# Optimization experiments

Measured on AMD Instinct MI355X. Metric: run time of the kernel, lower is better.

Reference implementation:

```python
import jax, jax.numpy as jnp
from jax import lax
import numpy as np

# pywt db4 filter bank (ascending order)
DEC_LO = np.array([-0.010597401784997278, 0.032883011666982945, 0.030841381835986965,
                   -0.18703481171888114, -0.02798376941698385, 0.6308807679295904,
                   0.7148465705525415, 0.23037781330885523], dtype=np.float32)
F_LEN = DEC_LO.shape[0]
_signs = ((-1.0) ** (np.arange(F_LEN) + 1)).astype(np.float32)
DEC_HI = _signs * DEC_LO[::-1]
REC_LO = DEC_LO[::-1].copy()
REC_HI = DEC_HI[::-1].copy()
# conv filters flipped -> cross-correlation kernels for lax.conv
DEC_K = np.stack([DEC_LO[::-1], DEC_HI[::-1]])[:, None, :]   # (2, 1, F): lo/hi analysis
REC_K = np.stack([REC_LO[::-1], REC_HI[::-1]])[None, :, :]   # (1, 2, F): synthesis, sums lo+hi
LEVELS = 3


def dwt_level(x, dec_k):
    """One symmetric-mode DWT level. x: (M, n) -> (cA, cD) each (M, floor((n+F-1)/2))."""
    f = dec_k.shape[-1]
    x_ext = jnp.pad(x, ((0, 0), (f - 1, f - 1)), mode='symmetric')[:, 1:]
    y = lax.conv_general_dilated(x_ext[:, None, :], dec_k, (2,), 'VALID',
                                 dimension_numbers=('NCH', 'OIH', 'NCH'))
    return y[:, 0], y[:, 1]


def idwt_level(ca, cd, rec_k, out_len):
    """One IDWT level; trims to out_len (original length at that level)."""
    f = rec_k.shape[-1]
    m, L = ca.shape
    up = jnp.zeros((m, 2, 2 * L), ca.dtype).at[:, 0, ::2].set(ca).at[:, 1, ::2].set(cd)
    y = lax.conv_general_dilated(up, rec_k, (1,), [(f - 1, f - 1)],
                                 dimension_numbers=('NCH', 'OIH', 'NCH'))[:, 0]
    s = f - 2
    return y[:, s:s + out_len]


def setup_inputs() -> dict:
    key = jax.random.key(0)
    B, N, D = 8, 4096, 768
    x = jax.random.normal(key, (B, N, D), dtype=jnp.float32)
    w_approx = jnp.ones((D,), dtype=jnp.float32)
    w_details = jnp.ones((LEVELS, D), dtype=jnp.float32)
    return {"x": x, "w_approx": w_approx, "w_details": w_details}


def reference(x, w_approx, w_details):
    B, N, D = x.shape
    dec_k = jnp.asarray(DEC_K)
    rec_k = jnp.asarray(REC_K)
    # all channels processed at once: (B, N, D) -> (B*D, N)
    sig = x.transpose(0, 2, 1).reshape(B * D, N)
    # J-level decomposition, recording per-level lengths for reconstruction
    a = sig
    lengths = []
    details = []
    for _ in range(LEVELS):
        lengths.append(a.shape[-1])
        a, d = dwt_level(a, dec_k)
        details.append(d)
    # pointwise mixing: one scalar per channel per band (matches ones(1,1,D) param sliced per-channel)
    def chan(w):  # (D,) -> (B*D, 1)
        return jnp.broadcast_to(w, (B, D)).reshape(B * D, 1)
    a = a * chan(w_approx)
    details = [d * chan(w_details[j]) for j, d in enumerate(details)]
    # reconstruction
    rec = a
    for j in reversed(range(LEVELS)):
        rec = idwt_level(rec, details[j], rec_k, lengths[j])
    rec = rec.reshape(B, D, N).transpose(0, 2, 1)
    # residual connection (dropout=0.0)
    return x + rec
```

## Files before the change

### kernel.cpp

```cpp
#include <hip/hip_runtime.h>


namespace {

constexpr int NT  = 256;
constexpr int N0  = 4096;
constexpr int DCH = 768;
constexpr int G   = 8;
constexpr int T   = 256;
constexpr int NTI = N0 / T;
constexpr int NDG = DCH / G;
constexpr int L1v = 2051, L2v = 1029, L3v = 518;

constexpr int SP   = 972;
constexpr int OX   = 0;
constexpr int OA1  = 356;
constexpr int OD1  = 536;
constexpr int OA2  = 716;
constexpr int OD2  = 804;
constexpr int OA3  = 892;
constexpr int OD3  = 932;
constexpr int OREC = 716;

__device__ constexpr float LO[8] = {
  -0.010597401784997278f,  0.032883011666982945f,  0.030841381835986965f,
  -0.18703481171888114f,  -0.02798376941698385f,   0.6308807679295904f,
   0.7148465705525415f,    0.23037781330885523f };
__device__ constexpr float HI[8] = {
  -0.23037781330885523f,   0.7148465705525415f,   -0.6308807679295904f,
  -0.02798376941698385f,   0.18703481171888114f,   0.030841381835986965f,
  -0.032883011666982945f, -0.010597401784997278f };
__device__ constexpr float LOF[8] = {
   0.23037781330885523f,   0.7148465705525415f,    0.6308807679295904f,
  -0.02798376941698385f,  -0.18703481171888114f,   0.030841381835986965f,
   0.032883011666982945f, -0.010597401784997278f };
__device__ constexpr float HIF[8] = {
  -0.010597401784997278f, -0.032883011666982945f,  0.030841381835986965f,
   0.18703481171888114f,  -0.02798376941698385f,  -0.6308807679295904f,
   0.7148465705525415f,   -0.23037781330885523f };

__device__ __forceinline__ int refl(int g, int n) {
  g = (g < 0) ? (-g - 1) : g;
  return (g >= n) ? (2 * n - 1 - g) : g;
}


template <int K>
__device__ __forceinline__ void analyze_v(const float* __restrict__ in,
                                          float* __restrict__ oa,
                                          float* __restrict__ od,
                                          int ntask, int i2) {
  for (int v = i2; v < ntask; v += 32) {
    float r[12];
#pragma unroll
    for (int j = 0; j < 3; ++j) {
      const float4 t = *reinterpret_cast<const float4*>(in + 4 * v + 4 * j);
      r[4 * j + 0] = t.x; r[4 * j + 1] = t.y;
      r[4 * j + 2] = t.z; r[4 * j + 3] = t.w;
    }
    float a0 = 0.f, h0 = 0.f, a1 = 0.f, h1 = 0.f;
#pragma unroll
    for (int k = 0; k < 8; ++k) {
      a0 = fmaf(LOF[k], r[K + k], a0);
      h0 = fmaf(HIF[k], r[K + k], h0);
      a1 = fmaf(LOF[k], r[K + 2 + k], a1);
      h1 = fmaf(HIF[k], r[K + 2 + k], h1);
    }
    *reinterpret_cast<float2*>(oa + 2 * v) = make_float2(a0, a1);
    *reinterpret_cast<float2*>(od + 2 * v) = make_float2(h0, h1);
  }
}

__device__ __forceinline__ void synth3_v(const float* __restrict__ pa,
                                         const float* __restrict__ pd,
                                         float* __restrict__ o, float sa,
                                         float sd, int ntask, int i2) {
  if (i2 < ntask) {
    const int u = i2;
    float ra[8], rd[8];
#pragma unroll
    for (int j = 0; j < 2; ++j) {
      const float4 t0 = *reinterpret_cast<const float4*>(pa + 4 * u + 4 * j);
      const float4 t1 = *reinterpret_cast<const float4*>(pd + 4 * u + 4 * j);
      ra[4*j+0] = t0.x; ra[4*j+1] = t0.y; ra[4*j+2] = t0.z; ra[4*j+3] = t0.w;
      rd[4*j+0] = t1.x; rd[4*j+1] = t1.y; rd[4*j+2] = t1.z; rd[4*j+3] = t1.w;
    }
    float ov[8];
#pragma unroll
    for (int tt = 0; tt < 4; ++tt) {
      float e = 0.f, ed = 0.f, oe = 0.f, od_ = 0.f;
#pragma unroll
      for (int m = 0; m < 4; ++m) {
        e   = fmaf(LO[2 * m + 1], ra[tt + m], e);
        ed  = fmaf(HI[2 * m + 1], rd[tt + m], ed);
        oe  = fmaf(LO[2 * m],     ra[tt + m], oe);
        od_ = fmaf(HI[2 * m],     rd[tt + m], od_);
      }
      ov[2 * tt]     = sa * e  + sd * ed;
      ov[2 * tt + 1] = sa * oe + sd * od_;
    }
    *reinterpret_cast<float4*>(o + 8 * u)     = make_float4(ov[0], ov[1], ov[2], ov[3]);
    *reinterpret_cast<float4*>(o + 8 * u + 4) = make_float4(ov[4], ov[5], ov[6], ov[7]);
  }
}

__device__ __forceinline__ void synth2_v(const float* __restrict__ pa,
                                         const float* __restrict__ pd,
                                         float* __restrict__ o, float sd,
                                         int ntask, int i2) {
  if (i2 < ntask) {
    const int u = i2;
    float ra[8], rd[12];
#pragma unroll
    for (int j = 0; j < 2; ++j) {
      const float4 t0 = *reinterpret_cast<const float4*>(pa + 4 * u + 4 * j);
      ra[4*j+0] = t0.x; ra[4*j+1] = t0.y; ra[4*j+2] = t0.z; ra[4*j+3] = t0.w;
    }
#pragma unroll
    for (int j = 0; j < 3; ++j) {
      const float4 t1 = *reinterpret_cast<const float4*>(pd + 4 * u + 4 + 4 * j);
      rd[4*j+0] = t1.x; rd[4*j+1] = t1.y; rd[4*j+2] = t1.z; rd[4*j+3] = t1.w;
    }
    float ov[8];
#pragma unroll
    for (int tt = 0; tt < 4; ++tt) {
      float e = 0.f, ed = 0.f, oe = 0.f, od_ = 0.f;
#pragma unroll
      for (int m = 0; m < 4; ++m) {
        e   = fmaf(LO[2 * m + 1], ra[tt + m], e);
        ed  = fmaf(HI[2 * m + 1], rd[tt + 2 + m], ed);
        oe  = fmaf(LO[2 * m],     ra[tt + m], oe);
        od_ = fmaf(HI[2 * m],     rd[tt + 2 + m], od_);
      }
      ov[2 * tt]     = e  + sd * ed;
      ov[2 * tt + 1] = oe + sd * od_;
    }
    *reinterpret_cast<float4*>(o + 8 * u)     = make_float4(ov[0], ov[1], ov[2], ov[3]);
    *reinterpret_cast<float4*>(o + 8 * u + 4) = make_float4(ov[4], ov[5], ov[6], ov[7]);
  }
}

__device__ __forceinline__ void final_v(const float* __restrict__ pa,
                                        const float* __restrict__ pd,
                                        const float* __restrict__ px,
                                        float* __restrict__ rec, float sd,
                                        int i2) {
  const int u = i2;
  float ra[8], rd[8], rx[12];
#pragma unroll
  for (int j = 0; j < 2; ++j) {
    const float4 t0 = *reinterpret_cast<const float4*>(pa + 4 * u + 4 * j);
    const float4 t1 = *reinterpret_cast<const float4*>(pd + 4 * u + 20 + 4 * j);
    ra[4*j+0] = t0.x; ra[4*j+1] = t0.y; ra[4*j+2] = t0.z; ra[4*j+3] = t0.w;
    rd[4*j+0] = t1.x; rd[4*j+1] = t1.y; rd[4*j+2] = t1.z; rd[4*j+3] = t1.w;
  }
#pragma unroll
  for (int j = 0; j < 3; ++j) {
    const float4 t2 = *reinterpret_cast<const float4*>(px + 8 * u + 44 + 4 * j);
    rx[4*j+0] = t2.x; rx[4*j+1] = t2.y; rx[4*j+2] = t2.z; rx[4*j+3] = t2.w;
  }
  float ov[8];
#pragma unroll
  for (int tt = 0; tt < 4; ++tt) {
    float e = 0.f, ed = 0.f, oe = 0.f, od_ = 0.f;
#pragma unroll
    for (int m = 0; m < 4; ++m) {
      e   = fmaf(LO[2 * m + 1], ra[tt + m], e);
      ed  = fmaf(HI[2 * m + 1], rd[tt + m], ed);
      oe  = fmaf(LO[2 * m],     ra[tt + m], oe);
      od_ = fmaf(HI[2 * m],     rd[tt + m], od_);
    }
    ov[2 * tt]     = e  + sd * ed  + rx[2 + 2 * tt];
    ov[2 * tt + 1] = oe + sd * od_ + rx[3 + 2 * tt];
  }
  *reinterpret_cast<float4*>(rec + 8 * u)     = make_float4(ov[0], ov[1], ov[2], ov[3]);
  *reinterpret_cast<float4*>(rec + 8 * u + 4) = make_float4(ov[4], ov[5], ov[6], ov[7]);
}


__device__ void analyze_g(const float* __restrict__ in, int Oin,
                          float* __restrict__ oa, float* __restrict__ od,
                          int cnt, int Oout, int lenout, int i2) {
  for (int p = i2; p < cnt; p += 32) {
    const int gp = refl(Oout + p, lenout);
    const int qb = 2 * gp - 6 - Oin;
    float alo = 0.f, ahi = 0.f;
#pragma unroll
    for (int k = 0; k < 8; ++k) {
      const float v = in[qb + k];
      alo = fmaf(LOF[k], v, alo);
      ahi = fmaf(HIF[k], v, ahi);
    }
    oa[p] = alo;
    od[p] = ahi;
  }
}

__device__ void synth_g(const float* __restrict__ ca,
                        const float* __restrict__ cd, int doff,
                        float* __restrict__ o, float sa, float sd, int npair,
                        int i2) {
  for (int t = i2; t < npair; t += 32) {
    float e = 0.f, ed = 0.f, oe = 0.f, od_ = 0.f;
#pragma unroll
    for (int m = 0; m < 4; ++m) {
      e   = fmaf(LO[2 * m + 1], ca[t + m], e);
      ed  = fmaf(HI[2 * m + 1], cd[t + doff + m], ed);
      oe  = fmaf(LO[2 * m],     ca[t + m], oe);
      od_ = fmaf(HI[2 * m],     cd[t + doff + m], od_);
    }
    o[2 * t]     = sa * e  + sd * ed;
    o[2 * t + 1] = sa * oe + sd * od_;
  }
}

}

__global__ __launch_bounds__(NT) void wavemix_kernel(
    const float* __restrict__ x, const float* __restrict__ wap,
    const float* __restrict__ wdet, float* __restrict__ out) {
  __shared__ float pool[G * SP];

  const int cpx = gridDim.x >> 3;
  const int wg  = (blockIdx.x & 7) * cpx + (blockIdx.x >> 3);
  const int nt   = wg & (NTI - 1);
  const int rest = wg >> 4;
  const int dg   = rest % NDG;
  const int b    = rest / NDG;
  const int n0   = nt * T;
  const int d0   = dg * G;
  const int tid  = threadIdx.x;
  const bool edge = (nt == 0) || (nt == NTI - 1);

  {
    const int q  = tid & 1;
    const int pl = tid >> 1;
    for (int p = pl; p < 352; p += 128) {
      int g = n0 - 46 + p;
      if (edge) g = refl(g, N0);
      const float4 v = *reinterpret_cast<const float4*>(
          x + ((size_t)b * N0 + g) * DCH + d0 + 4 * q);
      float* dst = pool + (4 * q) * SP + OX + p;
      dst[0]      = v.x;
      dst[SP]     = v.y;
      dst[2 * SP] = v.z;
      dst[3 * SP] = v.w;
    }
  }

  const int c2 = tid >> 5;
  const int i2 = tid & 31;
  float* P = pool + c2 * SP;
  const float wa = wap[d0 + c2];
  const float w2 = wdet[2 * DCH + d0 + c2];
  const float w1 = wdet[1 * DCH + d0 + c2];
  const float w0 = wdet[0 * DCH + d0 + c2];
  __syncthreads();

  if (!edge) {
    analyze_v<0>(P + OX,  P + OA1, P + OD1, 86, i2);
    __syncthreads();
    analyze_v<2>(P + OA1, P + OA2, P + OD2, 44, i2);
    __syncthreads();
    analyze_v<0>(P + OA2, P + OA3, P + OD3, 20, i2);
    __syncthreads();
    synth3_v(P + OA3, P + OD3, P + OA2, wa, w2, 9, i2);
    __syncthreads();
    synth2_v(P + OA2, P + OD2, P + OA1, w1, 17, i2);
    __syncthreads();
    final_v(P + OA1, P + OD1, P + OX, P + OREC, w0, i2);
  } else {
    analyze_g(P + OX,  n0 - 46,      P + OA1, P + OD1, 172, n0 / 2 - 20, L1v, i2);
    __syncthreads();
    analyze_g(P + OA1, n0 / 2 - 20,  P + OA2, P + OD2,  82, n0 / 4 - 6,  L2v, i2);
    __syncthreads();
    analyze_g(P + OA2, n0 / 4 - 6,   P + OA3, P + OD3,  38, n0 / 8,      L3v, i2);
    __syncthreads();
    synth_g(P + OA3, P + OD3, 0, P + OA2, wa,  w2, 35, i2);
    __syncthreads();
    synth_g(P + OA2, P + OD2, 6, P + OA1, 1.f, w1, 66, i2);
    __syncthreads();
    for (int t = i2; t < 128; t += 32) {
      const float* pa = P + OA1;
      const float* pd = P + OD1;
      float e = 0.f, ed = 0.f, oe = 0.f, od_ = 0.f;
#pragma unroll
      for (int m = 0; m < 4; ++m) {
        e   = fmaf(LO[2 * m + 1], pa[t + m], e);
        ed  = fmaf(HI[2 * m + 1], pd[t + 20 + m], ed);
        oe  = fmaf(LO[2 * m],     pa[t + m], oe);
        od_ = fmaf(HI[2 * m],     pd[t + 20 + m], od_);
      }
      (P + OREC)[2 * t]     = e  + w0 * ed  + (P + OX)[2 * t + 46];
      (P + OREC)[2 * t + 1] = oe + w0 * od_ + (P + OX)[2 * t + 47];
    }
  }
  __syncthreads();

  {
    const int c = tid & 7;
    const int j = tid >> 3;
    const float* R = pool + c * SP + OREC;
    float* orow = out + ((size_t)b * N0 + n0) * DCH + d0 + c;
    for (int pos = j; pos < T; pos += 32)
      orow[(size_t)pos * DCH] = R[pos];
  }
}

extern "C" void kernel_launch(void* const* d_in, const int* in_sizes, int n_in,
                              void* d_out, int out_size, void* d_ws, size_t ws_size,
                              hipStream_t stream) {
  const float* x  = (const float*)d_in[0];
  const float* wa = (const float*)d_in[1];
  const float* wd = (const float*)d_in[2];
  float* out      = (float*)d_out;

  const int B    = in_sizes[0] / (N0 * DCH);
  const int grid = B * NDG * NTI;
  wavemix_kernel<<<grid, NT, 0, stream>>>(x, wa, wd, out);
}
```

Before: 61.45 us.

## Replace shared-memory interior tiles with per-thread streaming register DWT pipeline

Interior tiles now give each thread one channel and stream along the sequence through a register-resident multi-level wavelet pipeline. Each thread reads x and writes out with coalesced stride-DCH accesses across threads, with no shared memory or barriers. Only the edge tiles keep the old shared-memory path. The change removes the halo recomputation and synchronisation cost, but the grid for interior work drops to 336 blocks. That reduces parallelism, and each thread carries a long serial dependency chain and heavy register use.

```diff
diff --git a/kernel.cpp b/kernel.cpp
--- a/kernel.cpp
+++ b/kernel.cpp
@@ -6,21 +6,16 @@
 constexpr int NT  = 256;
 constexpr int N0  = 4096;
 constexpr int DCH = 768;
+constexpr int T   = 256;
 constexpr int G   = 8;
-constexpr int T   = 256;
-constexpr int NTI = N0 / T;
 constexpr int NDG = DCH / G;
 constexpr int L1v = 2051, L2v = 1029, L3v = 518;
 
-constexpr int SP   = 972;
-constexpr int OX   = 0;
-constexpr int OA1  = 356;
-constexpr int OD1  = 536;
-constexpr int OA2  = 716;
-constexpr int OD2  = 804;
-constexpr int OA3  = 892;
-constexpr int OD3  = 932;
-constexpr int OREC = 716;
+constexpr int NINT = 8 * 14 * 3;
+
+constexpr int SP = 972;
+constexpr int OX = 0, OA1 = 356, OD1 = 536, OA2 = 716, OD2 = 804,
+              OA3 = 892, OD3 = 932, OREC = 716;
 
 __device__ constexpr float LO[8] = {
   -0.010597401784997278f,  0.032883011666982945f,  0.030841381835986965f,
@@ -44,137 +39,125 @@
   return (g >= n) ? (2 * n - 1 - g) : g;
 }
 
-
-template <int K>
-__device__ __forceinline__ void analyze_v(const float* __restrict__ in,
-                                          float* __restrict__ oa,
-                                          float* __restrict__ od,
-                                          int ntask, int i2) {
-  for (int v = i2; v < ntask; v += 32) {
-    float r[12];
-#pragma unroll
-    for (int j = 0; j < 3; ++j) {
-      const float4 t = *reinterpret_cast<const float4*>(in + 4 * v + 4 * j);
-      r[4 * j + 0] = t.x; r[4 * j + 1] = t.y;
-      r[4 * j + 2] = t.z; r[4 * j + 3] = t.w;
-    }
-    float a0 = 0.f, h0 = 0.f, a1 = 0.f, h1 = 0.f;
-#pragma unroll
-    for (int k = 0; k < 8; ++k) {
-      a0 = fmaf(LOF[k], r[K + k], a0);
-      h0 = fmaf(HIF[k], r[K + k], h0);
-      a1 = fmaf(LOF[k], r[K + 2 + k], a1);
-      h1 = fmaf(HIF[k], r[K + 2 + k], h1);
-    }
-    *reinterpret_cast<float2*>(oa + 2 * v) = make_float2(a0, a1);
-    *reinterpret_cast<float2*>(od + 2 * v) = make_float2(h0, h1);
+struct Streams {
+  float xa[22];
+  float a1a[14], d1a[29];
+  float a2a[10], d2a[13];
+  float a3a[5],  d3a[5];
+  float r2a[7],  r1a[11];
+};
+
+template <int SMODE>
+__device__ __forceinline__ void superstep(Streams& S,
+                                          const float* __restrict__ xrow,
+                                          float* __restrict__ orow, int bk8,
+                                          float wa, float w0, float w1,
+                                          float w2) {
+#pragma unroll
+  for (int i = 0; i < 16; ++i)
+    S.xa[6 + i] = xrow[(long)(bk8 - 48 + i) * DCH];
+
+#pragma unroll
+  for (int u = 0; u < 2; ++u) {
+#pragma unroll
+    for (int j = 0; j < 4; ++j) {
+      float slo = 0.f, shi = 0.f;
+#pragma unroll
+      for (int k = 0; k < 8; ++k) {
+        const float v = S.xa[8 * u + 2 * j + k];
+        slo = fmaf(LOF[k], v, slo);
+        shi = fmaf(HIF[k], v, shi);
+      }
+      S.a1a[6 + 4 * u + j]  = slo;
+      S.d1a[21 + 4 * u + j] = w0 * shi;
+    }
+#pragma unroll
+    for (int i = 0; i < 2; ++i) {
+      float slo = 0.f, shi = 0.f;
+#pragma unroll
+      for (int k = 0; k < 8; ++k) {
+        const float v = S.a1a[4 * u + 2 * i + k];
+        slo = fmaf(LOF[k], v, slo);
+        shi = fmaf(HIF[k], v, shi);
+      }
+      S.a2a[6 + 2 * u + i] = slo;
+      S.d2a[9 + 2 * u + i] = w1 * shi;
+    }
+    {
+      float slo = 0.f, shi = 0.f;
+#pragma unroll
+      for (int k = 0; k < 8; ++k) {
+        const float v = S.a2a[2 * u + k];
+        slo = fmaf(LOF[k], v, slo);
+        shi = fmaf(HIF[k], v, shi);
+      }
+      S.a3a[3 + u] = wa * slo;
+      S.d3a[3 + u] = w2 * shi;
+    }
+    {
+      float e = 0.f, o = 0.f;
+#pragma unroll
+      for (int m = 0; m < 4; ++m) {
+        e = fmaf(LO[2 * m + 1], S.a3a[u + m], e);
+        e = fmaf(HI[2 * m + 1], S.d3a[u + m], e);
+        o = fmaf(LO[2 * m],     S.a3a[u + m], o);
+        o = fmaf(HI[2 * m],     S.d3a[u + m], o);
+      }
+      S.r2a[3 + 2 * u]     = e;
+      S.r2a[3 + 2 * u + 1] = o;
+    }
+#pragma unroll
+    for (int h = 0; h < 2; ++h) {
+      float e = 0.f, o = 0.f;
+#pragma unroll
+      for (int m = 0; m < 4; ++m) {
+        e = fmaf(LO[2 * m + 1], S.r2a[2 * u + h + m], e);
+        e = fmaf(HI[2 * m + 1], S.d2a[2 * u + h + m], e);
+        o = fmaf(LO[2 * m],     S.r2a[2 * u + h + m], o);
+        o = fmaf(HI[2 * m],     S.d2a[2 * u + h + m], o);
+      }
+      S.r1a[3 + 4 * u + 2 * h]     = e;
+      S.r1a[3 + 4 * u + 2 * h + 1] = o;
+    }
+    if (SMODE != 0) {
+#pragma unroll
+      for (int tau = 0; tau < 4; ++tau) {
+        bool doSt;
+        if (SMODE == 2)      doSt = true;
+        else if (SMODE == 1) doSt = (u == 1) && (tau >= 1);
+        else                 doSt = (u == 0) || (tau == 0);
+        if (doSt) {
+          float e = 0.f, o = 0.f;
+#pragma unroll
+          for (int m = 0; m < 4; ++m) {
+            e = fmaf(LO[2 * m + 1], S.r1a[4 * u + tau + m], e);
+            e = fmaf(HI[2 * m + 1], S.d1a[4 * u + tau + m], e);
+            o = fmaf(LO[2 * m],     S.r1a[4 * u + tau + m], o);
+            o = fmaf(HI[2 * m],     S.d1a[4 * u + tau + m], o);
+          }
+          const long ofs = bk8 + 8 * u - 90 + 2 * tau;
+          orow[ofs * DCH]       = e + xrow[ofs * DCH];
+          orow[(ofs + 1) * DCH] = o + xrow[(ofs + 1) * DCH];
+        }
+      }
+    }
   }
-}
-
-__device__ __forceinline__ void synth3_v(const float* __restrict__ pa,
-                                         const float* __restrict__ pd,
-                                         float* __restrict__ o, float sa,
-                                         float sd, int ntask, int i2) {
-  if (i2 < ntask) {
-    const int u = i2;
-    float ra[8], rd[8];
-#pragma unroll
-    for (int j = 0; j < 2; ++j) {
-      const float4 t0 = *reinterpret_cast<const float4*>(pa + 4 * u + 4 * j);
-      const float4 t1 = *reinterpret_cast<const float4*>(pd + 4 * u + 4 * j);
-      ra[4*j+0] = t0.x; ra[4*j+1] = t0.y; ra[4*j+2] = t0.z; ra[4*j+3] = t0.w;
-      rd[4*j+0] = t1.x; rd[4*j+1] = t1.y; rd[4*j+2] = t1.z; rd[4*j+3] = t1.w;
-    }
-    float ov[8];
-#pragma unroll
-    for (int tt = 0; tt < 4; ++tt) {
-      float e = 0.f, ed = 0.f, oe = 0.f, od_ = 0.f;
-#pragma unroll
-      for (int m = 0; m < 4; ++m) {
-        e   = fmaf(LO[2 * m + 1], ra[tt + m], e);
-        ed  = fmaf(HI[2 * m + 1], rd[tt + m], ed);
-        oe  = fmaf(LO[2 * m],     ra[tt + m], oe);
-        od_ = fmaf(HI[2 * m],     rd[tt + m], od_);
-      }
-      ov[2 * tt]     = sa * e  + sd * ed;
-      ov[2 * tt + 1] = sa * oe + sd * od_;
-    }
-    *reinterpret_cast<float4*>(o + 8 * u)     = make_float4(ov[0], ov[1], ov[2], ov[3]);
-    *reinterpret_cast<float4*>(o + 8 * u + 4) = make_float4(ov[4], ov[5], ov[6], ov[7]);
-  }
-}
-
-__device__ __forceinline__ void synth2_v(const float* __restrict__ pa,
-                                         const float* __restrict__ pd,
-                                         float* __restrict__ o, float sd,
-                                         int ntask, int i2) {
-  if (i2 < ntask) {
-    const int u = i2;
-    float ra[8], rd[12];
-#pragma unroll
-    for (int j = 0; j < 2; ++j) {
-      const float4 t0 = *reinterpret_cast<const float4*>(pa + 4 * u + 4 * j);
-      ra[4*j+0] = t0.x; ra[4*j+1] = t0.y; ra[4*j+2] = t0.z; ra[4*j+3] = t0.w;
-    }
-#pragma unroll
-    for (int j = 0; j < 3; ++j) {
-      const float4 t1 = *reinterpret_cast<const float4*>(pd + 4 * u + 4 + 4 * j);
-      rd[4*j+0] = t1.x; rd[4*j+1] = t1.y; rd[4*j+2] = t1.z; rd[4*j+3] = t1.w;
-    }
-    float ov[8];
-#pragma unroll
-    for (int tt = 0; tt < 4; ++tt) {
-      float e = 0.f, ed = 0.f, oe = 0.f, od_ = 0.f;
-#pragma unroll
-      for (int m = 0; m < 4; ++m) {
-        e   = fmaf(LO[2 * m + 1], ra[tt + m], e);
-        ed  = fmaf(HI[2 * m + 1], rd[tt + 2 + m], ed);
-        oe  = fmaf(LO[2 * m],     ra[tt + m], oe);
-        od_ = fmaf(HI[2 * m],     rd[tt + 2 + m], od_);
-      }
-      ov[2 * tt]     = e  + sd * ed;
-      ov[2 * tt + 1] = oe + sd * od_;
-    }
-    *reinterpret_cast<float4*>(o + 8 * u)     = make_float4(ov[0], ov[1], ov[2], ov[3]);
-    *reinterpret_cast<float4*>(o + 8 * u + 4) = make_float4(ov[4], ov[5], ov[6], ov[7]);
-  }
-}
-
-__device__ __forceinline__ void final_v(const float* __restrict__ pa,
-                                        const float* __restrict__ pd,
-                                        const float* __restrict__ px,
-                                        float* __restrict__ rec, float sd,
-                                        int i2) {
-  const int u = i2;
-  float ra[8], rd[8], rx[12];
-#pragma unroll
-  for (int j = 0; j < 2; ++j) {
-    const float4 t0 = *reinterpret_cast<const float4*>(pa + 4 * u + 4 * j);
-    const float4 t1 = *reinterpret_cast<const float4*>(pd + 4 * u + 20 + 4 * j);
-    ra[4*j+0] = t0.x; ra[4*j+1] = t0.y; ra[4*j+2] = t0.z; ra[4*j+3] = t0.w;
-    rd[4*j+0] = t1.x; rd[4*j+1] = t1.y; rd[4*j+2] = t1.z; rd[4*j+3] = t1.w;
-  }
-#pragma unroll
-  for (int j = 0; j < 3; ++j) {
-    const float4 t2 = *reinterpret_cast<const float4*>(px + 8 * u + 44 + 4 * j);
-    rx[4*j+0] = t2.x; rx[4*j+1] = t2.y; rx[4*j+2] = t2.z; rx[4*j+3] = t2.w;
-  }
-  float ov[8];
-#pragma unroll
-  for (int tt = 0; tt < 4; ++tt) {
-    float e = 0.f, ed = 0.f, oe = 0.f, od_ = 0.f;
-#pragma unroll
-    for (int m = 0; m < 4; ++m) {
-      e   = fmaf(LO[2 * m + 1], ra[tt + m], e);
-      ed  = fmaf(HI[2 * m + 1], rd[tt + m], ed);
-      oe  = fmaf(LO[2 * m],     ra[tt + m], oe);
-      od_ = fmaf(HI[2 * m],     rd[tt + m], od_);
-    }
-    ov[2 * tt]     = e  + sd * ed  + rx[2 + 2 * tt];
-    ov[2 * tt + 1] = oe + sd * od_ + rx[3 + 2 * tt];
-  }
-  *reinterpret_cast<float4*>(rec + 8 * u)     = make_float4(ov[0], ov[1], ov[2], ov[3]);
-  *reinterpret_cast<float4*>(rec + 8 * u + 4) = make_float4(ov[4], ov[5], ov[6], ov[7]);
+#pragma unroll
+  for (int i = 0; i < 6; ++i)  S.xa[i]  = S.xa[i + 16];
+#pragma unroll
+  for (int i = 0; i < 6; ++i)  S.a1a[i] = S.a1a[i + 8];
+#pragma unroll
+  for (int i = 0; i < 21; ++i) S.d1a[i] = S.d1a[i + 8];
+#pragma unroll
+  for (int i = 0; i < 6; ++i)  S.a2a[i] = S.a2a[i + 4];
+#pragma unroll
+  for (int i = 0; i < 9; ++i)  S.d2a[i] = S.d2a[i + 4];
+#pragma unroll
+  for (int i = 0; i < 3; ++i) { S.a3a[i] = S.a3a[i + 2]; S.d3a[i] = S.d3a[i + 2]; }
+#pragma unroll
+  for (int i = 0; i < 3; ++i)  S.r2a[i] = S.r2a[i + 4];
+#pragma unroll
+  for (int i = 0; i < 3; ++i)  S.r1a[i] = S.r1a[i + 8];
 }
 
 
@@ -220,61 +203,79 @@
     const float* __restrict__ x, const float* __restrict__ wap,
     const float* __restrict__ wdet, float* __restrict__ out) {
   __shared__ float pool[G * SP];
-
-  const int cpx = gridDim.x >> 3;
-  const int wg  = (blockIdx.x & 7) * cpx + (blockIdx.x >> 3);
-  const int nt   = wg & (NTI - 1);
-  const int rest = wg >> 4;
-  const int dg   = rest % NDG;
-  const int b    = rest / NDG;
-  const int n0   = nt * T;
-  const int d0   = dg * G;
-  const int tid  = threadIdx.x;
-  const bool edge = (nt == 0) || (nt == NTI - 1);
-
-  {
-    const int q  = tid & 1;
-    const int pl = tid >> 1;
-    for (int p = pl; p < 352; p += 128) {
-      int g = n0 - 46 + p;
-      if (edge) g = refl(g, N0);
-      const float4 v = *reinterpret_cast<const float4*>(
-          x + ((size_t)b * N0 + g) * DCH + d0 + 4 * q);
-      float* dst = pool + (4 * q) * SP + OX + p;
-      dst[0]      = v.x;
-      dst[SP]     = v.y;
-      dst[2 * SP] = v.z;
-      dst[3 * SP] = v.w;
-    }
-  }
-
-  const int c2 = tid >> 5;
-  const int i2 = tid & 31;
-  float* P = pool + c2 * SP;
-  const float wa = wap[d0 + c2];
-  const float w2 = wdet[2 * DCH + d0 + c2];
-  const float w1 = wdet[1 * DCH + d0 + c2];
-  const float w0 = wdet[0 * DCH + d0 + c2];
-  __syncthreads();
-
-  if (!edge) {
-    analyze_v<0>(P + OX,  P + OA1, P + OD1, 86, i2);
-    __syncthreads();
-    analyze_v<2>(P + OA1, P + OA2, P + OD2, 44, i2);
-    __syncthreads();
-    analyze_v<0>(P + OA2, P + OA3, P + OD3, 20, i2);
-    __syncthreads();
-    synth3_v(P + OA3, P + OD3, P + OA2, wa, w2, 9, i2);
-    __syncthreads();
-    synth2_v(P + OA2, P + OD2, P + OA1, w1, 17, i2);
-    __syncthreads();
-    final_v(P + OA1, P + OD1, P + OX, P + OREC, w0, i2);
+  const int blk = blockIdx.x;
+  const int tid = threadIdx.x;
+
+  if (blk < NINT) {
+    const int wgroup = blk % 3;
+    const int rest   = blk / 3;
+    const int s      = 1 + rest % 14;
+    const int b      = rest / 14;
+    const int n0     = s * T;
+    const int d      = wgroup * 256 + tid;
+
+    const float* __restrict__ xrow = x   + ((size_t)b * N0 + n0) * DCH + d;
+    float* __restrict__       orow = out + ((size_t)b * N0 + n0) * DCH + d;
+    const float wa = wap[d];
+    const float w0 = wdet[d];
+    const float w1 = wdet[DCH + d];
+    const float w2 = wdet[2 * DCH + d];
+
+    Streams S = {};
+    int bk8 = 0;
+#pragma unroll 1
+    for (int m = 0; m < 5; ++m) {
+      superstep<0>(S, xrow, orow, bk8, wa, w0, w1, w2);
+      bk8 += 16;
+    }
+    superstep<1>(S, xrow, orow, bk8, wa, w0, w1, w2);
+    bk8 += 16;
+#pragma unroll 1
+    for (int m = 0; m < 15; ++m) {
+      superstep<2>(S, xrow, orow, bk8, wa, w0, w1, w2);
+      bk8 += 16;
+    }
+    superstep<3>(S, xrow, orow, bk8, wa, w0, w1, w2);
   } else {
-    analyze_g(P + OX,  n0 - 46,      P + OA1, P + OD1, 172, n0 / 2 - 20, L1v, i2);
-    __syncthreads();
-    analyze_g(P + OA1, n0 / 2 - 20,  P + OA2, P + OD2,  82, n0 / 4 - 6,  L2v, i2);
-    __syncthreads();
-    analyze_g(P + OA2, n0 / 4 - 6,   P + OA3, P + OD3,  38, n0 / 8,      L3v, i2);
+    const int e    = blk - NINT;
+    const int nt   = (e & 1) ? 15 : 0;
+    const int rest = e >> 1;
+    const int dg   = rest % NDG;
+    const int b    = rest / NDG;
+    const int n0   = nt * T;
+    const int d0   = dg * G;
+
+    const size_t base = (size_t)b * N0 * DCH + d0;
+
+    {
+      const int q  = tid & 1;
+      const int pl = tid >> 1;
+      for (int p = pl; p < 352; p += 128) {
+        const int g = refl(n0 - 46 + p, N0);
+        const float4 v = *reinterpret_cast<const float4*>(
+            x + ((size_t)b * N0 + g) * DCH + d0 + 4 * q);
+        float* dst = pool + (4 * q) * SP + OX + p;
+        dst[0]      = v.x;
+        dst[SP]     = v.y;
+        dst[2 * SP] = v.z;
+        dst[3 * SP] = v.w;
+      }
+    }
+
+    const int c2 = tid >> 5;
+    const int i2 = tid & 31;
+    float* P = pool + c2 * SP;
+    const float wa = wap[d0 + c2];
+    const float w2 = wdet[2 * DCH + d0 + c2];
+    const float w1 = wdet[1 * DCH + d0 + c2];
+    const float w0 = wdet[0 * DCH + d0 + c2];
+    __syncthreads();
+
+    analyze_g(P + OX,  n0 - 46,     P + OA1, P + OD1, 172, n0 / 2 - 20, L1v, i2);
+    __syncthreads();
+    analyze_g(P + OA1, n0 / 2 - 20, P + OA2, P + OD2,  82, n0 / 4 - 6,  L2v, i2);
+    __syncthreads();
+    analyze_g(P + OA2, n0 / 4 - 6,  P + OA3, P + OD3,  38, n0 / 8,      L3v, i2);
     __syncthreads();
     synth_g(P + OA3, P + OD3, 0, P + OA2, wa,  w2, 35, i2);
     __syncthreads();
@@ -283,27 +284,27 @@
     for (int t = i2; t < 128; t += 32) {
       const float* pa = P + OA1;
       const float* pd = P + OD1;
-      float e = 0.f, ed = 0.f, oe = 0.f, od_ = 0.f;
+      float e2 = 0.f, ed = 0.f, oe = 0.f, od_ = 0.f;
 #pragma unroll
       for (int m = 0; m < 4; ++m) {
-        e   = fmaf(LO[2 * m + 1], pa[t + m], e);
+        e2  = fmaf(LO[2 * m + 1], pa[t + m], e2);
         ed  = fmaf(HI[2 * m + 1], pd[t + 20 + m], ed);
         oe  = fmaf(LO[2 * m],     pa[t + m], oe);
         od_ = fmaf(HI[2 * m],     pd[t + 20 + m], od_);
       }
-      (P + OREC)[2 * t]     = e  + w0 * ed  + (P + OX)[2 * t + 46];
+      (P + OREC)[2 * t]     = e2 + w0 * ed  + (P + OX)[2 * t + 46];
       (P + OREC)[2 * t + 1] = oe + w0 * od_ + (P + OX)[2 * t + 47];
     }
-  }
-  __syncthreads();
-
-  {
-    const int c = tid & 7;
-    const int j = tid >> 3;
-    const float* R = pool + c * SP + OREC;
-    float* orow = out + ((size_t)b * N0 + n0) * DCH + d0 + c;
-    for (int pos = j; pos < T; pos += 32)
-      orow[(size_t)pos * DCH] = R[pos];
+    __syncthreads();
+
+    {
+      const int c = tid & 7;
+      const int j = tid >> 3;
+      const float* R = pool + c * SP + OREC;
+      float* orow = out + ((size_t)b * N0 + n0) * DCH + d0 + c;
+      for (int pos = j; pos < T; pos += 32)
+        orow[(size_t)pos * DCH] = R[pos];
+    }
   }
 }
 
@@ -315,7 +316,6 @@
   const float* wd = (const float*)d_in[2];
   float* out      = (float*)d_out;
 
-  const int B    = in_sizes[0] / (N0 * DCH);
-  const int grid = B * NDG * NTI;
+  const int grid = NINT + 8 * NDG * 2;
   wavemix_kernel<<<grid, NT, 0, stream>>>(x, wa, wd, out);
 }
```

Result: no change. 61.79 us (+0.5%).
